# Performance work log

Measured on AMD Instinct MI355X. Metric: run time of the kernel, lower is better.

## Reference

```python
import jax, jax.numpy as jnp
import numpy as np

N_NODES = 100000
N_EDGES = 1600000
IN_DIM = 128
HID_DIM = 128
OUT_DIM = 16
N_GRAPHS = 128


def setup_inputs() -> dict:
    key = jax.random.key(0)
    ks = jax.random.split(key, 8)
    x = jax.random.normal(ks[0], (N_NODES, IN_DIM), dtype=jnp.float32)
    edge_index = jax.random.randint(ks[1], (2, N_EDGES), 0, N_NODES, dtype=jnp.int64)
    batch = jnp.sort(jax.random.randint(ks[2], (N_NODES,), 0, N_GRAPHS, dtype=jnp.int64))
    # GCNConv params (glorot-ish scale) and Linear params
    w1 = jax.random.normal(ks[3], (IN_DIM, HID_DIM), dtype=jnp.float32) / np.sqrt(IN_DIM)
    b1 = jnp.zeros((HID_DIM,), dtype=jnp.float32)
    w2 = jax.random.normal(ks[4], (HID_DIM, HID_DIM), dtype=jnp.float32) / np.sqrt(HID_DIM)
    b2 = jnp.zeros((HID_DIM,), dtype=jnp.float32)
    wc = jax.random.normal(ks[5], (HID_DIM, OUT_DIM), dtype=jnp.float32) / np.sqrt(HID_DIM)
    bc = jnp.zeros((OUT_DIM,), dtype=jnp.float32)
    return {"x": x, "edge_index": edge_index, "batch": batch,
            "w1": w1, "b1": b1, "w2": w2, "b2": b2, "wc": wc, "bc": bc}


def _gcn_layer(h, src, dst, w, b, n_nodes):
    # h: [N, Fin]; src/dst: [E+N] (self-loops already appended)
    h = h @ w  # [N, Fout]
    ones = jnp.ones_like(dst, dtype=h.dtype)
    deg = jax.ops.segment_sum(ones, dst, num_segments=n_nodes)  # [N]
    dinv = jnp.where(deg > 0, jax.lax.rsqrt(deg), 0.0)
    norm = dinv[src] * dinv[dst]  # [E+N]
    msg = h[src] * norm[:, None]  # gather + scale, [E+N, Fout]
    out = jax.ops.segment_sum(msg, dst, num_segments=n_nodes)  # scatter-add
    return out + b


def reference(x, edge_index, batch, w1, b1, w2, b2, wc, bc):
    n = x.shape[0]
    loop = jnp.arange(n, dtype=edge_index.dtype)
    src = jnp.concatenate([edge_index[0], loop])  # add self-loops (PyG default)
    dst = jnp.concatenate([edge_index[1], loop])

    h = jax.nn.relu(_gcn_layer(x, src, dst, w1, b1, n))
    h = jax.nn.relu(_gcn_layer(h, src, dst, w2, b2, n))

    # global mean pool over graphs
    sums = jax.ops.segment_sum(h, batch, num_segments=N_GRAPHS)  # [G, H]
    cnt = jax.ops.segment_sum(jnp.ones((n,), h.dtype), batch, num_segments=N_GRAPHS)
    pooled = sums / jnp.maximum(cnt, 1.0)[:, None]

    return pooled @ wc + bc  # [G, OUT_DIM]
```

## Files before the change

kernel.cpp:

```cpp
#include <hip/hip_runtime.h>
#include <stdint.h>

#define NN 100000
#define NE 1600000
#define FDIM 128
#define NGRAPH 128
#define ODIM 16
#define NBKT 391
#define CAP 4608
#define SCHUNK 8192
#define NSCAT ((NE + SCHUNK - 1) / SCHUNK)
#define NSTARTB ((NN + 255) / 256)

typedef __attribute__((ext_vector_type(8))) short short8;
typedef __attribute__((ext_vector_type(8))) unsigned short ushort8;
typedef __attribute__((ext_vector_type(4))) float f32x4;

__device__ __forceinline__ float blo(unsigned int p) { return __uint_as_float(p << 16); }
__device__ __forceinline__ float bhi(unsigned int p) { return __uint_as_float(p & 0xffff0000u); }
__device__ __forceinline__ unsigned short f2b(float f) {
    unsigned int u = __float_as_uint(f);
    unsigned int r = (u + 0x7fffu + ((u >> 16) & 1u)) >> 16;
    return (unsigned short)r;
}
__device__ __forceinline__ unsigned int packbf(float lo, float hi) {
    return (unsigned int)f2b(lo) | ((unsigned int)f2b(hi) << 16);
}

__device__ __forceinline__ int detect_w(const int* __restrict__ ei) {
    int lane = threadIdx.x & 63;
    int v = ei[2 * lane + 1];
    return (__ballot(v != 0) == 0ULL) ? 1 : 0;
}
__device__ __forceinline__ int ld_idx(const int* __restrict__ p, long long i, int w) {
    return w ? p[2 * i] : p[i];
}

__global__ void __launch_bounds__(256) k_prep(
    const float* __restrict__ w1, const float* __restrict__ w2,
    unsigned short* __restrict__ wt1, unsigned short* __restrict__ wt2,
    const int* __restrict__ ei, const int* __restrict__ batch,
    int* __restrict__ gstart, int* __restrict__ bcursor,
    unsigned short* __restrict__ xws)
{
    int b = blockIdx.x, t = threadIdx.x;
    if (b < 128) {
        int idx = b * 256 + t;
        int which = idx >> 14, r = idx & 16383;
        int k = r >> 7, j = r & 127;
        const float* w = which ? w2 : w1;
        unsigned short* wt = which ? wt2 : wt1;
        wt[j * 128 + k] = f2b(w[k * 128 + j]);
    } else if (b < 128 + NSTARTB) {
        int w = detect_w(ei);
        int i = (b - 128) * 256 + t;
        if (i < NN) {
            int bb = ld_idx(batch, i, w);
            int prev = (i == 0) ? -1 : ld_idx(batch, i - 1, w);
            for (int g = prev + 1; g <= bb; ++g) gstart[g] = i;
            if (i == NN - 1)
                for (int g = bb + 1; g <= NGRAPH; ++g) gstart[g] = NN;
        }
    } else {
        int i = (b - 128 - NSTARTB) * 256 + t;
        if (i < NBKT) bcursor[i] = i * CAP;
        if (b == 128 + NSTARTB && t < FDIM) xws[(size_t)NN * FDIM + t] = 0;
    }
}

__global__ void __launch_bounds__(512) k_scat(const int* __restrict__ ei,
                                              int* __restrict__ bcursor,
                                              unsigned int* __restrict__ rec) {
    __shared__ int hist[NBKT];
    __shared__ int gbase[NBKT];
    __shared__ int lcur[NBKT];
    int t = threadIdx.x;
    int w = detect_w(ei);
    for (int i = t; i < NBKT; i += 512) hist[i] = 0;
    __syncthreads();
    long long e0 = (long long)blockIdx.x * SCHUNK;
    unsigned int myrec[16];
    int mybkt[16];
    #pragma unroll
    for (int j = 0; j < 16; ++j) {
        long long e = e0 + j * 512 + t;
        if (e < NE) {
            int s = ld_idx(ei, e, w);
            int d = ld_idx(ei, NE + e, w);
            mybkt[j] = d >> 8;
            myrec[j] = (unsigned int)s | ((unsigned int)(d & 255) << 17);
            atomicAdd(&hist[mybkt[j]], 1);
        } else mybkt[j] = -1;
    }
    __syncthreads();
    for (int i = t; i < NBKT; i += 512) {
        int c = hist[i];
        gbase[i] = c ? atomicAdd(&bcursor[i], c) : 0;
        lcur[i] = 0;
    }
    __syncthreads();
    #pragma unroll
    for (int j = 0; j < 16; ++j) {
        int b = mybkt[j];
        if (b >= 0) {
            int r = atomicAdd(&lcur[b], 1);
            int p = gbase[b] + r;
            if (p < (b + 1) * CAP) rec[p] = myrec[j];
        }
    }
}

__global__ void __launch_bounds__(256) k_bucket(const unsigned int* __restrict__ rec,
                                                const int* __restrict__ bcursor,
                                                int* __restrict__ csr,
                                                int* __restrict__ offs,
                                                int* __restrict__ deg,
                                                float* __restrict__ dinv) {
    __shared__ unsigned int rbuf[CAP];
    __shared__ int srcout[CAP];
    __shared__ int hist[256], scn[256], cur[256];
    int b = blockIdx.x, t = threadIdx.x;
    int base = b * CAP;
    int cnt = bcursor[b] - base;
    if (cnt > CAP) cnt = CAP;
    hist[t] = 0;
    __syncthreads();
    for (int j = t; j < cnt; j += 256) {
        unsigned int r = rec[base + j];
        rbuf[j] = r;
        atomicAdd(&hist[r >> 17], 1);
    }
    __syncthreads();
    int v = hist[t];
    scn[t] = v;
    __syncthreads();
    for (int o = 1; o < 256; o <<= 1) {
        int tv = (t >= o) ? scn[t - o] : 0;
        __syncthreads();
        scn[t] += tv;
        __syncthreads();
    }
    int excl = scn[t] - v;
    cur[t] = excl;
    int node = (b << 8) + t;
    if (node < NN) {
        offs[node] = base + excl;
        deg[node] = v;
        dinv[node] = rsqrtf((float)(v + 1));
    }
    __syncthreads();
    for (int j = t; j < cnt; j += 256) {
        unsigned int r = rbuf[j];
        int p = atomicAdd(&cur[r >> 17], 1);
        srcout[p] = (int)(r & 0x1FFFFu);
    }
    __syncthreads();
    for (int j = t; j < cnt; j += 256) csr[base + j] = srcout[j];
}

#define LWS 136
template <bool BF16IN>
__global__ void __launch_bounds__(256) k_gemm(
    const void* __restrict__ Xv,
    const unsigned short* __restrict__ WT,
    const float* __restrict__ dinv,
    unsigned short* __restrict__ OUT)
{
    __shared__ unsigned short lw[128 * LWS];
    int tid = threadIdx.x;
    for (int it = 0; it < 8; ++it) {
        int vidx = it * 256 + tid;
        int j = vidx >> 4, kc = vidx & 15;
        ushort8 v = *(const ushort8*)(WT + j * 128 + kc * 8);
        *(ushort8*)(&lw[j * LWS + kc * 8]) = v;
    }
    __syncthreads();

    int wave = tid >> 6, lane = tid & 63;
    int quad = lane >> 4, n16 = lane & 15;
    int row0 = (blockIdx.x * 4 + wave) * 16;
    if (row0 >= NN) return;

    f32x4 acc[8];
    for (int ct = 0; ct < 8; ++ct) acc[ct] = (f32x4){0.f, 0.f, 0.f, 0.f};

    const int arow = row0 + n16;
    for (int kk = 0; kk < 4; ++kk) {
        short8 a;
        if (BF16IN) {
            a = *(const short8*)((const unsigned short*)Xv + (size_t)arow * 128 + kk * 32 + quad * 8);
        } else {
            const float* ap = (const float*)Xv + (size_t)arow * 128 + kk * 32 + quad * 8;
            float4 a01 = *(const float4*)(ap);
            float4 a23 = *(const float4*)(ap + 4);
            a[0] = (short)f2b(a01.x); a[1] = (short)f2b(a01.y);
            a[2] = (short)f2b(a01.z); a[3] = (short)f2b(a01.w);
            a[4] = (short)f2b(a23.x); a[5] = (short)f2b(a23.y);
            a[6] = (short)f2b(a23.z); a[7] = (short)f2b(a23.w);
        }
        for (int ct = 0; ct < 8; ++ct) {
            short8 b = *(const short8*)(&lw[(ct * 16 + n16) * LWS + kk * 32 + quad * 8]);
            acc[ct] = __builtin_amdgcn_mfma_f32_16x16x32_bf16(a, b, acc[ct], 0, 0, 0);
        }
    }
    for (int r = 0; r < 4; ++r) {
        int row = row0 + quad * 4 + r;
        float dv = dinv[row];
        for (int ct = 0; ct < 8; ++ct)
            OUT[(size_t)row * 128 + ct * 16 + n16] = f2b(acc[ct][r] * dv);
    }
}

__global__ void __launch_bounds__(256) k_agg(
    const unsigned short* __restrict__ XWS,
    const int* __restrict__ csr,
    const int* __restrict__ offs,
    const int* __restrict__ deg,
    const float* __restrict__ dinv,
    const float* __restrict__ bias,
    unsigned short* __restrict__ H)
{
    int wave = threadIdx.x >> 6, lane = threadIdx.x & 63;
    int v = blockIdx.x * 4 + wave;
    int g = lane >> 4, f = lane & 15;
    int beg = offs[v], end = beg + deg[v];
    float a[8];
    {
        uint4 q = *(const uint4*)(XWS + (size_t)v * FDIM + f * 8);
        float m = (g == 0) ? 1.f : 0.f;
        a[0] = m * blo(q.x); a[1] = m * bhi(q.x); a[2] = m * blo(q.y); a[3] = m * bhi(q.y);
        a[4] = m * blo(q.z); a[5] = m * bhi(q.z); a[6] = m * blo(q.w); a[7] = m * bhi(q.w);
    }
    int e1 = end - 1;
    for (int j = beg; j < end; j += 16) {
        int j0 = j + g, j1 = j + 4 + g, j2 = j + 8 + g, j3 = j + 12 + g;
        int i0 = csr[j0 < end ? j0 : e1]; i0 = (j0 < end) ? i0 : NN;
        int i1 = csr[j1 < end ? j1 : e1]; i1 = (j1 < end) ? i1 : NN;
        int i2 = csr[j2 < end ? j2 : e1]; i2 = (j2 < end) ? i2 : NN;
        int i3 = csr[j3 < end ? j3 : e1]; i3 = (j3 < end) ? i3 : NN;
        uint4 q0 = *(const uint4*)(XWS + (size_t)i0 * FDIM + f * 8);
        uint4 q1 = *(const uint4*)(XWS + (size_t)i1 * FDIM + f * 8);
        uint4 q2 = *(const uint4*)(XWS + (size_t)i2 * FDIM + f * 8);
        uint4 q3 = *(const uint4*)(XWS + (size_t)i3 * FDIM + f * 8);
        a[0] += blo(q0.x); a[1] += bhi(q0.x); a[2] += blo(q0.y); a[3] += bhi(q0.y);
        a[4] += blo(q0.z); a[5] += bhi(q0.z); a[6] += blo(q0.w); a[7] += bhi(q0.w);
        a[0] += blo(q1.x); a[1] += bhi(q1.x); a[2] += blo(q1.y); a[3] += bhi(q1.y);
        a[4] += blo(q1.z); a[5] += bhi(q1.z); a[6] += blo(q1.w); a[7] += bhi(q1.w);
        a[0] += blo(q2.x); a[1] += bhi(q2.x); a[2] += blo(q2.y); a[3] += bhi(q2.y);
        a[4] += blo(q2.z); a[5] += bhi(q2.z); a[6] += blo(q2.w); a[7] += bhi(q2.w);
        a[0] += blo(q3.x); a[1] += bhi(q3.x); a[2] += blo(q3.y); a[3] += bhi(q3.y);
        a[4] += blo(q3.z); a[5] += bhi(q3.z); a[6] += blo(q3.w); a[7] += bhi(q3.w);
    }
    #pragma unroll
    for (int i = 0; i < 8; ++i) {
        a[i] += __shfl_xor(a[i], 16);
        a[i] += __shfl_xor(a[i], 32);
    }
    if (g == 0) {
        float dv = dinv[v];
        float4 b0 = *(const float4*)(bias + f * 8);
        float4 b1 = *(const float4*)(bias + f * 8 + 4);
        uint4 o;
        o.x = packbf(fmaxf(fmaf(a[0], dv, b0.x), 0.f), fmaxf(fmaf(a[1], dv, b0.y), 0.f));
        o.y = packbf(fmaxf(fmaf(a[2], dv, b0.z), 0.f), fmaxf(fmaf(a[3], dv, b0.w), 0.f));
        o.z = packbf(fmaxf(fmaf(a[4], dv, b1.x), 0.f), fmaxf(fmaf(a[5], dv, b1.y), 0.f));
        o.w = packbf(fmaxf(fmaf(a[6], dv, b1.z), 0.f), fmaxf(fmaf(a[7], dv, b1.w), 0.f));
        *(uint4*)(H + (size_t)v * FDIM + f * 8) = o;
    }
}

__global__ void __launch_bounds__(256) k_poolcls(
    const unsigned short* __restrict__ H, const int* __restrict__ gstart,
    const float* __restrict__ wc, const float* __restrict__ bc,
    float* __restrict__ out)
{
    __shared__ float red[512];
    __shared__ float pl[FDIM];
    int g = blockIdx.x;
    int t = threadIdx.x;
    int pair = t & 63;
    int seg = t >> 6;
    int beg = gstart[g], end = gstart[g + 1];
    float a0 = 0.f, a1 = 0.f;
    for (int i = beg + seg; i < end; i += 4) {
        unsigned int q = *(const unsigned int*)(H + (size_t)i * FDIM + 2 * pair);
        a0 += blo(q); a1 += bhi(q);
    }
    red[t] = a0; red[256 + t] = a1;
    __syncthreads();
    if (seg == 0) {
        a0 = red[t] + red[t + 64] + red[t + 128] + red[t + 192];
        a1 = red[256 + t] + red[256 + t + 64] + red[256 + t + 128] + red[256 + t + 192];
        float inv = 1.f / fmaxf((float)(end - beg), 1.f);
        pl[2 * pair] = a0 * inv;
        pl[2 * pair + 1] = a1 * inv;
    }
    __syncthreads();
    int o = t & 15, fs = t >> 4;
    float acc = 0.f;
    #pragma unroll
    for (int k = 0; k < 8; ++k)
        acc += pl[fs * 8 + k] * wc[(fs * 8 + k) * ODIM + o];
    red[t] = acc;
    __syncthreads();
    if (t < 16) {
        float s = bc[t];
        #pragma unroll
        for (int k = 0; k < 16; ++k) s += red[k * 16 + t];
        out[g * ODIM + t] = s;
    }
}

extern "C" void kernel_launch(void* const* d_in, const int* in_sizes, int n_in,
                              void* d_out, int out_size, void* d_ws, size_t ws_size,
                              hipStream_t stream) {
    const float* x   = (const float*)d_in[0];
    const int* ei    = (const int*)d_in[1];
    const int* batch = (const int*)d_in[2];
    const float* w1  = (const float*)d_in[3];
    const float* b1  = (const float*)d_in[4];
    const float* w2  = (const float*)d_in[5];
    const float* b2  = (const float*)d_in[6];
    const float* wc  = (const float*)d_in[7];
    const float* bc  = (const float*)d_in[8];
    float* out = (float*)d_out;

    char* ws = (char*)d_ws;
    size_t off = 0;
    auto alloc = [&](size_t bytes) -> void* {
        off = (off + 255) & ~(size_t)255;
        void* p = ws + off;
        off += bytes;
        return p;
    };
    int*   bcursor = (int*)alloc(NBKT * 4);
    int*   offs    = (int*)alloc(NN * 4);
    int*   deg     = (int*)alloc(NN * 4);
    float* dinv    = (float*)alloc(NN * 4);
    int*   gstart  = (int*)alloc((NGRAPH + 1) * 4);
    unsigned int* rec = (unsigned int*)alloc((size_t)NBKT * CAP * 4);
    int*   csr     = (int*)alloc((size_t)NBKT * CAP * 4 + 256);
    unsigned short* wt1 = (unsigned short*)alloc(128 * 128 * 2);
    unsigned short* wt2 = (unsigned short*)alloc(128 * 128 * 2);
    unsigned short* xws = (unsigned short*)alloc((size_t)(NN + 1) * FDIM * 2);
    unsigned short* h   = (unsigned short*)alloc((size_t)NN * FDIM * 2);

    k_prep<<<128 + NSTARTB + 2, 256, 0, stream>>>(w1, w2, wt1, wt2, ei, batch, gstart, bcursor, xws);
    k_scat<<<NSCAT, 512, 0, stream>>>(ei, bcursor, rec);
    k_bucket<<<NBKT, 256, 0, stream>>>(rec, bcursor, csr, offs, deg, dinv);

    k_gemm<false><<<(NN / 16 + 3) / 4, 256, 0, stream>>>(x, wt1, dinv, xws);
    k_agg<<<NN / 4, 256, 0, stream>>>(xws, csr, offs, deg, dinv, b1, h);
    k_gemm<true><<<(NN / 16 + 3) / 4, 256, 0, stream>>>(h, wt2, dinv, xws);
    k_agg<<<NN / 4, 256, 0, stream>>>(xws, csr, offs, deg, dinv, b2, h);
    k_poolcls<<<NGRAPH, 256, 0, stream>>>(h, gstart, wc, bc, out);
}
```

Baseline: 333.5 us.

## Pad CSR rows to multiples of 16 with pre-scaled byte offsets and self-loop

```diff
diff --git a/kernel.cpp b/kernel.cpp
--- a/kernel.cpp
+++ b/kernel.cpp
@@ -8,13 +8,15 @@
 #define ODIM 16
 #define NBKT 391
 #define CAP 4608
-#define SCHUNK 8192
+#define PCAP 8704
+#define SCHUNK 2048
 #define NSCAT ((NE + SCHUNK - 1) / SCHUNK)
 #define NSTARTB ((NN + 255) / 256)
 
 typedef __attribute__((ext_vector_type(8))) short short8;
 typedef __attribute__((ext_vector_type(8))) unsigned short ushort8;
 typedef __attribute__((ext_vector_type(4))) float f32x4;
+typedef __attribute__((ext_vector_type(2))) float f32x2;
 
 __device__ __forceinline__ float blo(unsigned int p) { return __uint_as_float(p << 16); }
 __device__ __forceinline__ float bhi(unsigned int p) { return __uint_as_float(p & 0xffff0000u); }
@@ -79,10 +81,10 @@
     for (int i = t; i < NBKT; i += 512) hist[i] = 0;
     __syncthreads();
     long long e0 = (long long)blockIdx.x * SCHUNK;
-    unsigned int myrec[16];
-    int mybkt[16];
+    unsigned int myrec[4];
+    int mybkt[4];
     #pragma unroll
-    for (int j = 0; j < 16; ++j) {
+    for (int j = 0; j < 4; ++j) {
         long long e = e0 + j * 512 + t;
         if (e < NE) {
             int s = ld_idx(ei, e, w);
@@ -100,7 +102,7 @@
     }
     __syncthreads();
     #pragma unroll
-    for (int j = 0; j < 16; ++j) {
+    for (int j = 0; j < 4; ++j) {
         int b = mybkt[j];
         if (b >= 0) {
             int r = atomicAdd(&lcur[b], 1);
@@ -117,22 +119,25 @@
                                                 int* __restrict__ deg,
                                                 float* __restrict__ dinv) {
     __shared__ unsigned int rbuf[CAP];
-    __shared__ int srcout[CAP];
+    __shared__ int srcout[PCAP];
     __shared__ int hist[256], scn[256], cur[256];
     int b = blockIdx.x, t = threadIdx.x;
-    int base = b * CAP;
-    int cnt = bcursor[b] - base;
+    int rbase = b * CAP;
+    int cnt = bcursor[b] - rbase;
     if (cnt > CAP) cnt = CAP;
     hist[t] = 0;
     __syncthreads();
     for (int j = t; j < cnt; j += 256) {
-        unsigned int r = rec[base + j];
+        unsigned int r = rec[rbase + j];
         rbuf[j] = r;
         atomicAdd(&hist[r >> 17], 1);
     }
-    __syncthreads();
+    for (int j = t; j < PCAP; j += 256) srcout[j] = NN << 8;
+    __syncthreads();
+    int node = (b << 8) + t;
     int v = hist[t];
-    scn[t] = v;
+    int pv = (node < NN) ? ((v + 16) & ~15) : 0;
+    scn[t] = pv;
     __syncthreads();
     for (int o = 1; o < 256; o <<= 1) {
         int tv = (t >= o) ? scn[t - o] : 0;
@@ -140,22 +145,24 @@
         scn[t] += tv;
         __syncthreads();
     }
-    int excl = scn[t] - v;
-    cur[t] = excl;
-    int node = (b << 8) + t;
+    int pexcl = scn[t] - pv;
+    cur[t] = pexcl;
+    int obase = b * PCAP;
     if (node < NN) {
-        offs[node] = base + excl;
-        deg[node] = v;
+        offs[node] = obase + pexcl;
+        deg[node] = pv;
         dinv[node] = rsqrtf((float)(v + 1));
+        srcout[pexcl + v] = node << 8;
     }
     __syncthreads();
     for (int j = t; j < cnt; j += 256) {
         unsigned int r = rbuf[j];
         int p = atomicAdd(&cur[r >> 17], 1);
-        srcout[p] = (int)(r & 0x1FFFFu);
-    }
-    __syncthreads();
-    for (int j = t; j < cnt; j += 256) csr[base + j] = srcout[j];
+        srcout[p] = (int)(r & 0x1FFFFu) << 8;
+    }
+    __syncthreads();
+    int total = scn[255];
+    for (int j = t; j < total; j += 256) csr[obase + j] = srcout[j];
 }
 
 #define LWS 136
@@ -211,6 +218,13 @@
     }
 }
 
+__device__ __forceinline__ void acc8(f32x2* a2, uint4 q) {
+    a2[0] += (f32x2){blo(q.x), bhi(q.x)};
+    a2[1] += (f32x2){blo(q.y), bhi(q.y)};
+    a2[2] += (f32x2){blo(q.z), bhi(q.z)};
+    a2[3] += (f32x2){blo(q.w), bhi(q.w)};
+}
+
 __global__ void __launch_bounds__(256) k_agg(
     const unsigned short* __restrict__ XWS,
     const int* __restrict__ csr,
@@ -223,48 +237,42 @@
     int wave = threadIdx.x >> 6, lane = threadIdx.x & 63;
     int v = blockIdx.x * 4 + wave;
     int g = lane >> 4, f = lane & 15;
-    int beg = offs[v], end = beg + deg[v];
-    float a[8];
-    {
-        uint4 q = *(const uint4*)(XWS + (size_t)v * FDIM + f * 8);
-        float m = (g == 0) ? 1.f : 0.f;
-        a[0] = m * blo(q.x); a[1] = m * bhi(q.x); a[2] = m * blo(q.y); a[3] = m * bhi(q.y);
-        a[4] = m * blo(q.z); a[5] = m * bhi(q.z); a[6] = m * blo(q.w); a[7] = m * bhi(q.w);
-    }
-    int e1 = end - 1;
-    for (int j = beg; j < end; j += 16) {
-        int j0 = j + g, j1 = j + 4 + g, j2 = j + 8 + g, j3 = j + 12 + g;
-        int i0 = csr[j0 < end ? j0 : e1]; i0 = (j0 < end) ? i0 : NN;
-        int i1 = csr[j1 < end ? j1 : e1]; i1 = (j1 < end) ? i1 : NN;
-        int i2 = csr[j2 < end ? j2 : e1]; i2 = (j2 < end) ? i2 : NN;
-        int i3 = csr[j3 < end ? j3 : e1]; i3 = (j3 < end) ? i3 : NN;
-        uint4 q0 = *(const uint4*)(XWS + (size_t)i0 * FDIM + f * 8);
-        uint4 q1 = *(const uint4*)(XWS + (size_t)i1 * FDIM + f * 8);
-        uint4 q2 = *(const uint4*)(XWS + (size_t)i2 * FDIM + f * 8);
-        uint4 q3 = *(const uint4*)(XWS + (size_t)i3 * FDIM + f * 8);
-        a[0] += blo(q0.x); a[1] += bhi(q0.x); a[2] += blo(q0.y); a[3] += bhi(q0.y);
-        a[4] += blo(q0.z); a[5] += bhi(q0.z); a[6] += blo(q0.w); a[7] += bhi(q0.w);
-        a[0] += blo(q1.x); a[1] += bhi(q1.x); a[2] += blo(q1.y); a[3] += bhi(q1.y);
-        a[4] += blo(q1.z); a[5] += bhi(q1.z); a[6] += blo(q1.w); a[7] += bhi(q1.w);
-        a[0] += blo(q2.x); a[1] += bhi(q2.x); a[2] += blo(q2.y); a[3] += bhi(q2.y);
-        a[4] += blo(q2.z); a[5] += bhi(q2.z); a[6] += blo(q2.w); a[7] += bhi(q2.w);
-        a[0] += blo(q3.x); a[1] += bhi(q3.x); a[2] += blo(q3.y); a[3] += bhi(q3.y);
-        a[4] += blo(q3.z); a[5] += bhi(q3.z); a[6] += blo(q3.w); a[7] += bhi(q3.w);
+    int beg = offs[v], pdeg = deg[v];
+    const char* xb = (const char*)XWS;
+    unsigned fo = (unsigned)(f * 16);
+    const int* cp = csr + beg + 4 * g;
+
+    f32x2 a2[4];
+    a2[0] = (f32x2){0.f, 0.f}; a2[1] = (f32x2){0.f, 0.f};
+    a2[2] = (f32x2){0.f, 0.f}; a2[3] = (f32x2){0.f, 0.f};
+
+    for (int j = 0; j < pdeg; j += 16) {
+        int4 c = *(const int4*)(cp + j);
+        uint4 q0 = *(const uint4*)(xb + ((unsigned)c.x + fo));
+        uint4 q1 = *(const uint4*)(xb + ((unsigned)c.y + fo));
+        uint4 q2 = *(const uint4*)(xb + ((unsigned)c.z + fo));
+        uint4 q3 = *(const uint4*)(xb + ((unsigned)c.w + fo));
+        acc8(a2, q0);
+        acc8(a2, q1);
+        acc8(a2, q2);
+        acc8(a2, q3);
     }
     #pragma unroll
-    for (int i = 0; i < 8; ++i) {
-        a[i] += __shfl_xor(a[i], 16);
-        a[i] += __shfl_xor(a[i], 32);
+    for (int i = 0; i < 4; ++i) {
+        a2[i].x += __shfl_xor(a2[i].x, 16);
+        a2[i].y += __shfl_xor(a2[i].y, 16);
+        a2[i].x += __shfl_xor(a2[i].x, 32);
+        a2[i].y += __shfl_xor(a2[i].y, 32);
     }
     if (g == 0) {
         float dv = dinv[v];
         float4 b0 = *(const float4*)(bias + f * 8);
         float4 b1 = *(const float4*)(bias + f * 8 + 4);
         uint4 o;
-        o.x = packbf(fmaxf(fmaf(a[0], dv, b0.x), 0.f), fmaxf(fmaf(a[1], dv, b0.y), 0.f));
-        o.y = packbf(fmaxf(fmaf(a[2], dv, b0.z), 0.f), fmaxf(fmaf(a[3], dv, b0.w), 0.f));
-        o.z = packbf(fmaxf(fmaf(a[4], dv, b1.x), 0.f), fmaxf(fmaf(a[5], dv, b1.y), 0.f));
-        o.w = packbf(fmaxf(fmaf(a[6], dv, b1.z), 0.f), fmaxf(fmaf(a[7], dv, b1.w), 0.f));
+        o.x = packbf(fmaxf(fmaf(a2[0].x, dv, b0.x), 0.f), fmaxf(fmaf(a2[0].y, dv, b0.y), 0.f));
+        o.y = packbf(fmaxf(fmaf(a2[1].x, dv, b0.z), 0.f), fmaxf(fmaf(a2[1].y, dv, b0.w), 0.f));
+        o.z = packbf(fmaxf(fmaf(a2[2].x, dv, b1.x), 0.f), fmaxf(fmaf(a2[2].y, dv, b1.y), 0.f));
+        o.w = packbf(fmaxf(fmaf(a2[3].x, dv, b1.z), 0.f), fmaxf(fmaf(a2[3].y, dv, b1.w), 0.f));
         *(uint4*)(H + (size_t)v * FDIM + f * 8) = o;
     }
 }
@@ -339,7 +347,7 @@
     float* dinv    = (float*)alloc(NN * 4);
     int*   gstart  = (int*)alloc((NGRAPH + 1) * 4);
     unsigned int* rec = (unsigned int*)alloc((size_t)NBKT * CAP * 4);
-    int*   csr     = (int*)alloc((size_t)NBKT * CAP * 4 + 256);
+    int*   csr     = (int*)alloc((size_t)NBKT * PCAP * 4 + 256);
     unsigned short* wt1 = (unsigned short*)alloc(128 * 128 * 2);
     unsigned short* wt2 = (unsigned short*)alloc(128 * 128 * 2);
     unsigned short* xws = (unsigned short*)alloc((size_t)(NN + 1) * FDIM * 2);
```

Result: slower. 342.3 us (+2.6%).
